# Kernel tuning notes

Hardware: AMD Instinct MI355X
Metric: run time of the kernel (lower is better)

The kernel has to match this reference:

```python
import math
import jax, jax.numpy as jnp
from jax import lax
import numpy as np

C_CURV = 0.01
CHUNK = 1024
EPS = 1e-15
TANH_CLIP = 1.0 - 1e-6


def safe_norm(x):
    return jnp.maximum(jnp.linalg.norm(x, axis=-1, keepdims=True), EPS)


def exp_map_zero(v, c):
    sqrt_c = math.sqrt(c)
    vn = safe_norm(v)
    return jnp.tanh(sqrt_c * vn) * v / (sqrt_c * vn)


def log_map_zero(y, c):
    sqrt_c = math.sqrt(c)
    yn = safe_norm(y)
    arg = jnp.clip(sqrt_c * yn, -TANH_CLIP, TANH_CLIP)
    return jnp.arctanh(arg) * y / (sqrt_c * yn)


def mobius_add(x, y, c):
    x2 = jnp.sum(x * x, axis=-1, keepdims=True)
    y2 = jnp.sum(y * y, axis=-1, keepdims=True)
    xy = jnp.sum(x * y, axis=-1, keepdims=True)
    num = (1.0 + 2.0 * c * xy + c * y2) * x + (1.0 - c * x2) * y
    den = 1.0 + 2.0 * c * xy + (c * c) * x2 * y2
    return num / jnp.maximum(den, EPS)


def givens_rotation(x, angles):
    # x: (B, d), angles: (B, d/2)
    x1 = x[:, 0::2]
    x2 = x[:, 1::2]
    cos_a = jnp.cos(angles)
    sin_a = jnp.sin(angles)
    out1 = cos_a * x1 - sin_a * x2
    out2 = sin_a * x1 + cos_a * x2
    # interleave back: stack on axis 2 then flatten
    return jnp.stack([out1, out2], axis=2).reshape(x.shape[0], x.shape[1])


def setup_inputs() -> dict:
    key = jax.random.key(0)
    k1, k2, k3, k4, k5, k6 = jax.random.split(key, 6)
    E, R, D, B = 40960, 480, 512, 128
    # keep entity points well inside the Poincare ball of curvature c
    entity_embedding = 0.05 * jax.random.normal(k1, (E, D), dtype=jnp.float32)
    rel_embedding = jax.random.normal(k2, (R, D), dtype=jnp.float32)  # unused, interface parity
    rel_rot = jax.random.uniform(k3, (R, D // 2), dtype=jnp.float32,
                                 minval=-math.pi, maxval=math.pi)
    rel_trans = jax.random.uniform(k4, (R, D), dtype=jnp.float32,
                                   minval=-0.001, maxval=0.001)
    entity_bias = jnp.zeros((E,), dtype=jnp.float32)
    triplets = jax.random.randint(k6, (B, 3), 0, R, dtype=jnp.int64)
    return {
        "entity_embedding": entity_embedding,
        "rel_embedding": rel_embedding,
        "rel_rot": rel_rot,
        "rel_trans": rel_trans,
        "entity_bias": entity_bias,
        "triplets": triplets,
    }


def reference(entity_embedding, rel_embedding, rel_rot, rel_trans, entity_bias, triplets):
    c = C_CURV
    E, D = entity_embedding.shape
    r_idx = triplets[:, 1]
    s_emb = entity_embedding[triplets[:, 0]]            # (B, d)
    s_tan = log_map_zero(s_emb, c)
    rot_s_tan = givens_rotation(s_tan, rel_rot[r_idx])
    rot_s = exp_map_zero(rot_s_tan, c)
    t_r = exp_map_zero(rel_trans[r_idx], c)
    query = mobius_add(rot_s, t_r, c)                   # (B, d)

    n_chunks = E // CHUNK
    ent_chunks = entity_embedding.reshape(n_chunks, CHUNK, D)
    bias_chunks = entity_bias.reshape(n_chunks, CHUNK)

    neg_q = -query[:, None, :]                          # (B, 1, d)

    def body(_, inp):
        cand, b = inp                                   # (CHUNK, d), (CHUNK,)
        diff = mobius_add(neg_q, cand[None, :, :], c)   # (B, CHUNK, d)
        dist_sq = jnp.sum(diff * diff, axis=-1)         # (B, CHUNK)
        return None, -dist_sq + b[None, :]

    _, chunks = lax.scan(body, None, (ent_chunks, bias_chunks))  # (n_chunks, B, CHUNK)
    scores = jnp.transpose(chunks, (1, 0, 2)).reshape(query.shape[0], E)
    scores = scores + entity_bias[triplets[:, 0]][:, None]
    return scores
```

## Files before the change

### kernel.cpp

```cpp
#include <hip/hip_runtime.h>
#include <math.h>

#define C_C   0.01f
#define SQC   0.1f
#define EPSF  1e-15f
#define TCLIP (1.0f - 1e-6f)

typedef short short8 __attribute__((ext_vector_type(8)));
typedef float f32x4  __attribute__((ext_vector_type(4)));

__device__ __forceinline__ float wred(float v) {
#pragma unroll
    for (int off = 32; off > 0; off >>= 1) v += __shfl_xor(v, off, 64);
    return v;
}

__device__ __forceinline__ float dot4(const float4& a, const float4& b) {
    return a.x * b.x + a.y * b.y + a.z * b.z + a.w * b.w;
}

__device__ __forceinline__ unsigned int f2bf(float f) {
    unsigned int u = __float_as_uint(f);
    u += 0x7fffu + ((u >> 16) & 1u);
    return u >> 16;
}
__device__ __forceinline__ unsigned int pk2(float a, float b) {
    return f2bf(a) | (f2bf(b) << 16);
}

__global__ __launch_bounds__(64)
void build_queries(const float* __restrict__ ent,
                   const float* __restrict__ rrot,
                   const float* __restrict__ rtrans,
                   const float* __restrict__ ebias,
                   const int* __restrict__ trip,
                   unsigned short* __restrict__ qb,
                   float* __restrict__ q2buf,
                   float* __restrict__ sbbuf)
{
    const int b    = blockIdx.x;
    const int lane = threadIdx.x;
    const int t0   = trip[b * 3 + 0];
    const int r    = trip[b * 3 + 1];

    const float* srow = ent + (size_t)t0 * 512;
    float4 s0 = *(const float4*)(srow + 4 * lane);
    float4 s1 = *(const float4*)(srow + 256 + 4 * lane);

    float ss = dot4(s0, s0) + dot4(s1, s1);
    ss = wred(ss);
    float yn  = fmaxf(sqrtf(ss), EPSF);
    float arg = fminf(SQC * yn, TCLIP);
    float fl  = atanhf(arg) / (SQC * yn);

    const float* arow = rrot + (size_t)r * 256;
    float2 a01 = *(const float2*)(arow + 2 * lane);
    float2 a23 = *(const float2*)(arow + 128 + 2 * lane);
    float c0, n0, c1, n1, c2, n2, c3, n3;
    sincosf(a01.x, &n0, &c0);
    sincosf(a01.y, &n1, &c1);
    sincosf(a23.x, &n2, &c2);
    sincosf(a23.y, &n3, &c3);

    float t0x = s0.x * fl, t0y = s0.y * fl, t0z = s0.z * fl, t0w = s0.w * fl;
    float t1x = s1.x * fl, t1y = s1.y * fl, t1z = s1.z * fl, t1w = s1.w * fl;

    float4 r0, r1;
    r0.x = c0 * t0x - n0 * t0y;  r0.y = n0 * t0x + c0 * t0y;
    r0.z = c1 * t0z - n1 * t0w;  r0.w = n1 * t0z + c1 * t0w;
    r1.x = c2 * t1x - n2 * t1y;  r1.y = n2 * t1x + c2 * t1y;
    r1.z = c3 * t1z - n3 * t1w;  r1.w = n3 * t1z + c3 * t1w;

    float vv = dot4(r0, r0) + dot4(r1, r1);
    vv = wred(vv);
    float vn = fmaxf(sqrtf(vv), EPSF);
    float fx = tanhf(SQC * vn) / (SQC * vn);

    const float* trow = rtrans + (size_t)r * 512;
    float4 u0 = *(const float4*)(trow + 4 * lane);
    float4 u1 = *(const float4*)(trow + 256 + 4 * lane);
    float tt = dot4(u0, u0) + dot4(u1, u1);
    float rt = dot4(r0, u0) + dot4(r1, u1);
    tt = wred(tt);
    rt = wred(rt);
    float tn = fmaxf(sqrtf(tt), EPSF);
    float fy = tanhf(SQC * tn) / (SQC * tn);

    float x2 = fx * fx * vv;
    float y2 = fy * fy * tt;
    float xy = fx * fy * rt;
    float ca  = 1.0f + 2.0f * C_C * xy + C_C * y2;
    float cb  = 1.0f - C_C * x2;
    float den = fmaxf(1.0f + 2.0f * C_C * xy + C_C * C_C * x2 * y2, EPSF);
    float inv = 1.0f / den;

    float4 q0, q1;
    q0.x = (ca * fx * r0.x + cb * fy * u0.x) * inv;
    q0.y = (ca * fx * r0.y + cb * fy * u0.y) * inv;
    q0.z = (ca * fx * r0.z + cb * fy * u0.z) * inv;
    q0.w = (ca * fx * r0.w + cb * fy * u0.w) * inv;
    q1.x = (ca * fx * r1.x + cb * fy * u1.x) * inv;
    q1.y = (ca * fx * r1.y + cb * fy * u1.y) * inv;
    q1.z = (ca * fx * r1.z + cb * fy * u1.z) * inv;
    q1.w = (ca * fx * r1.w + cb * fy * u1.w) * inv;

    float qq = dot4(q0, q0) + dot4(q1, q1);
    qq = wred(qq);

    unsigned short* qrow = qb + (size_t)b * 512;
    uint2 h0, h1;
    h0.x = pk2(q0.x, q0.y);  h0.y = pk2(q0.z, q0.w);
    h1.x = pk2(q1.x, q1.y);  h1.y = pk2(q1.z, q1.w);
    *(uint2*)(qrow + 4 * lane)       = h0;
    *(uint2*)(qrow + 256 + 4 * lane) = h1;
    if (lane == 0) {
        q2buf[b] = qq;
        sbbuf[b] = ebias[t0];
    }
}

__global__ __launch_bounds__(256)
void score_mfma(const float* __restrict__ ent,
                const float* __restrict__ ebias,
                const unsigned short* __restrict__ qb,
                const float* __restrict__ q2buf,
                const float* __restrict__ sbbuf,
                float* __restrict__ out, int E)
{
    __shared__ unsigned short qs[128 * 64];
    __shared__ unsigned short es[64 * 64];
    __shared__ float e2s[64];

    const int tid  = threadIdx.x;
    const int lane = tid & 63;
    const int wid  = tid >> 6;
    const int wr   = wid >> 1;
    const int wc   = wid & 1;
    const int e0   = blockIdx.x * 64;

    f32x4 acc[4][2];
#pragma unroll
    for (int mi = 0; mi < 4; ++mi)
#pragma unroll
        for (int nj = 0; nj < 2; ++nj) acc[mi][nj] = (f32x4)0.0f;

    const int erow0 = tid >> 3;
    const int ekc   = tid & 7;
    float e2p0 = 0.0f, e2p1 = 0.0f;

    for (int k0 = 0; k0 < 512; k0 += 64) {
        __syncthreads();
#pragma unroll
        for (int i = 0; i < 4; ++i) {
            int ci  = i * 256 + tid;
            int row = ci >> 3, kc = ci & 7;
            uint4 v = *(const uint4*)(qb + (size_t)row * 512 + k0 + kc * 8);
            int off = row * 128 + ((kc * 16) ^ ((row & 7) << 4));
            *(uint4*)((char*)qs + off) = v;
        }
        {
            const float* src = ent + (size_t)(e0 + erow0) * 512 + k0 + ekc * 8;
            float4 f0 = *(const float4*)(src);
            float4 f1 = *(const float4*)(src + 4);
            e2p0 += dot4(f0, f0) + dot4(f1, f1);
            uint4 p = { pk2(f0.x, f0.y), pk2(f0.z, f0.w),
                        pk2(f1.x, f1.y), pk2(f1.z, f1.w) };
            int off = erow0 * 128 + ((ekc * 16) ^ ((erow0 & 7) << 4));
            *(uint4*)((char*)es + off) = p;
        }
        {
            int row = erow0 + 32;
            const float* src = ent + (size_t)(e0 + row) * 512 + k0 + ekc * 8;
            float4 f0 = *(const float4*)(src);
            float4 f1 = *(const float4*)(src + 4);
            e2p1 += dot4(f0, f0) + dot4(f1, f1);
            uint4 p = { pk2(f0.x, f0.y), pk2(f0.z, f0.w),
                        pk2(f1.x, f1.y), pk2(f1.z, f1.w) };
            int off = row * 128 + ((ekc * 16) ^ ((row & 7) << 4));
            *(uint4*)((char*)es + off) = p;
        }
        __syncthreads();

#pragma unroll
        for (int ks = 0; ks < 2; ++ks) {
            const int kb = (ks * 32 + (lane >> 4) * 8) * 2;
            short8 a[4], bfr[2];
#pragma unroll
            for (int mi = 0; mi < 4; ++mi) {
                int row = wr * 64 + mi * 16 + (lane & 15);
                a[mi] = *(const short8*)((const char*)qs +
                         row * 128 + (kb ^ ((row & 7) << 4)));
            }
#pragma unroll
            for (int nj = 0; nj < 2; ++nj) {
                int row = wc * 32 + nj * 16 + (lane & 15);
                bfr[nj] = *(const short8*)((const char*)es +
                           row * 128 + (kb ^ ((row & 7) << 4)));
            }
#pragma unroll
            for (int mi = 0; mi < 4; ++mi)
#pragma unroll
                for (int nj = 0; nj < 2; ++nj)
                    acc[mi][nj] = __builtin_amdgcn_mfma_f32_16x16x32_bf16(
                        a[mi], bfr[nj], acc[mi][nj], 0, 0, 0);
        }
    }

    e2p0 += __shfl_xor(e2p0, 1, 64);
    e2p0 += __shfl_xor(e2p0, 2, 64);
    e2p0 += __shfl_xor(e2p0, 4, 64);
    e2p1 += __shfl_xor(e2p1, 1, 64);
    e2p1 += __shfl_xor(e2p1, 2, 64);
    e2p1 += __shfl_xor(e2p1, 4, 64);
    if ((tid & 7) == 0) {
        e2s[erow0]      = e2p0;
        e2s[erow0 + 32] = e2p1;
    }
    __syncthreads();

    float e2v[2], bev[2];
#pragma unroll
    for (int nj = 0; nj < 2; ++nj) {
        int ecol = wc * 32 + nj * 16 + (lane & 15);
        e2v[nj] = e2s[ecol];
        bev[nj] = ebias[e0 + ecol];
    }
#pragma unroll
    for (int mi = 0; mi < 4; ++mi) {
        const int qbase = wr * 64 + mi * 16 + (lane >> 4) * 4;
        float q2a[4], sba[4];
#pragma unroll
        for (int r = 0; r < 4; ++r) {
            q2a[r] = q2buf[qbase + r];
            sba[r] = sbbuf[qbase + r];
        }
#pragma unroll
        for (int nj = 0; nj < 2; ++nj) {
            const int ecol = e0 + wc * 32 + nj * 16 + (lane & 15);
            const float e2 = e2v[nj];
            const float be = bev[nj];
#pragma unroll
            for (int r = 0; r < 4; ++r) {
                float q2  = q2a[r];
                float xy  = -acc[mi][nj][r];
                float ca  = 1.0f + 2.0f * C_C * xy + C_C * e2;
                float cb  = 1.0f - C_C * q2;
                float den = fmaxf(1.0f + 2.0f * C_C * xy + C_C * C_C * q2 * e2, EPSF);
                float id2 = 1.0f / (den * den);
                float dist = (ca * ca * q2 + 2.0f * ca * cb * xy + cb * cb * e2) * id2;
                out[(size_t)(qbase + r) * E + ecol] = sba[r] + be - dist;
            }
        }
    }
}

extern "C" void kernel_launch(void* const* d_in, const int* in_sizes, int n_in,
                              void* d_out, int out_size, void* d_ws, size_t ws_size,
                              hipStream_t stream) {
    const float* ent    = (const float*)d_in[0];
    const float* rrot   = (const float*)d_in[2];
    const float* rtrans = (const float*)d_in[3];
    const float* ebias  = (const float*)d_in[4];
    const int*   trip   = (const int*)d_in[5];
    float* out = (float*)d_out;

    const int B = in_sizes[5] / 3;
    const int E = in_sizes[0] / 512;

    unsigned short* qb = (unsigned short*)d_ws;
    float* q2buf = (float*)(qb + (size_t)B * 512);
    float* sbbuf = q2buf + B;

    build_queries<<<B, 64, 0, stream>>>(ent, rrot, rtrans, ebias, trip,
                                        qb, q2buf, sbbuf);
    score_mfma<<<E / 64, 256, 0, stream>>>(ent, ebias, qb, q2buf, sbbuf, out, E);
}
```

Measured before the change: 145.5 us.

## Double-buffer LDS tiles with register prefetch and widen entity tile to 128

The scoring kernel now processes 128 entities per block instead of 64 and double-buffers the query and entity tiles in LDS. Global loads for the next K-slice are issued into registers before the MFMA work on the current slice, then stored to the alternate buffer. This halves redundant query tile loads and aims to hide global latency behind the matrix math. In exchange, LDS use and registers rise and the grid halves, which may reduce occupancy and CU fill.

```diff
diff --git a/kernel.cpp b/kernel.cpp
--- a/kernel.cpp
+++ b/kernel.cpp
@@ -127,101 +127,107 @@
                 const float* __restrict__ sbbuf,
                 float* __restrict__ out, int E)
 {
-    __shared__ unsigned short qs[128 * 64];
-    __shared__ unsigned short es[64 * 64];
-    __shared__ float e2s[64];
+    __shared__ unsigned short qs[2][128 * 64];
+    __shared__ unsigned short es[2][128 * 64];
+    __shared__ float e2s[128];
 
     const int tid  = threadIdx.x;
     const int lane = tid & 63;
     const int wid  = tid >> 6;
     const int wr   = wid >> 1;
     const int wc   = wid & 1;
-    const int e0   = blockIdx.x * 64;
-
-    f32x4 acc[4][2];
+    const int e0   = blockIdx.x * 128;
+
+    const int row  = tid >> 1;
+    const int half = tid & 1;
+
+    f32x4 acc[4][4];
 #pragma unroll
     for (int mi = 0; mi < 4; ++mi)
 #pragma unroll
-        for (int nj = 0; nj < 2; ++nj) acc[mi][nj] = (f32x4)0.0f;
-
-    const int erow0 = tid >> 3;
-    const int ekc   = tid & 7;
-    float e2p0 = 0.0f, e2p1 = 0.0f;
-
-    for (int k0 = 0; k0 < 512; k0 += 64) {
+        for (int nj = 0; nj < 4; ++nj) acc[mi][nj] = (f32x4)0.0f;
+
+    uint4  qreg[4];
+    float4 ereg[8];
+    float  e2p = 0.0f;
+
+    const unsigned short* qsrc0 = qb + (size_t)row * 512 + half * 32;
+    const float*          esrc0 = ent + (size_t)(e0 + row) * 512 + half * 32;
+
+#define LOAD_TILES(K0)                                                    \
+    {                                                                     \
+        const unsigned short* qsrc = qsrc0 + (K0);                        \
+        _Pragma("unroll")                                                 \
+        for (int c = 0; c < 4; ++c) qreg[c] = *(const uint4*)(qsrc + c * 8); \
+        const float* esrc = esrc0 + (K0);                                 \
+        _Pragma("unroll")                                                 \
+        for (int c = 0; c < 8; ++c) ereg[c] = *(const float4*)(esrc + c * 4); \
+    }
+
+#define STORE_TILES(BUF)                                                  \
+    {                                                                     \
+        _Pragma("unroll")                                                 \
+        for (int c = 0; c < 4; ++c) {                                     \
+            int off = row * 128 + ((((half * 4 + c) * 16)) ^ ((row & 7) << 4)); \
+            *(uint4*)((char*)qs[BUF] + off) = qreg[c];                    \
+        }                                                                 \
+        _Pragma("unroll")                                                 \
+        for (int p = 0; p < 4; ++p) {                                     \
+            float4 f0 = ereg[2 * p], f1 = ereg[2 * p + 1];                \
+            e2p += dot4(f0, f0) + dot4(f1, f1);                           \
+            uint4 pkd = { pk2(f0.x, f0.y), pk2(f0.z, f0.w),               \
+                          pk2(f1.x, f1.y), pk2(f1.z, f1.w) };             \
+            int off = row * 128 + ((((half * 4 + p) * 16)) ^ ((row & 7) << 4)); \
+            *(uint4*)((char*)es[BUF] + off) = pkd;                        \
+        }                                                                 \
+    }
+
+    LOAD_TILES(0);
+    STORE_TILES(0);
+    __syncthreads();
+
+    int cur = 0;
+#pragma unroll
+    for (int t = 0; t < 8; ++t) {
+        if (t < 7) LOAD_TILES((t + 1) * 64);
+
+#pragma unroll
+        for (int ks = 0; ks < 2; ++ks) {
+            const int kb = (ks * 4 + (lane >> 4)) * 16;
+            short8 a[4], b[4];
+#pragma unroll
+            for (int mi = 0; mi < 4; ++mi) {
+                int r = wr * 64 + mi * 16 + (lane & 15);
+                a[mi] = *(const short8*)((const char*)qs[cur] +
+                         r * 128 + (kb ^ ((r & 7) << 4)));
+            }
+#pragma unroll
+            for (int nj = 0; nj < 4; ++nj) {
+                int r = wc * 64 + nj * 16 + (lane & 15);
+                b[nj] = *(const short8*)((const char*)es[cur] +
+                         r * 128 + (kb ^ ((r & 7) << 4)));
+            }
+#pragma unroll
+            for (int mi = 0; mi < 4; ++mi)
+#pragma unroll
+                for (int nj = 0; nj < 4; ++nj)
+                    acc[mi][nj] = __builtin_amdgcn_mfma_f32_16x16x32_bf16(
+                        a[mi], b[nj], acc[mi][nj], 0, 0, 0);
+        }
+
+        if (t < 7) STORE_TILES(cur ^ 1);
         __syncthreads();
-#pragma unroll
-        for (int i = 0; i < 4; ++i) {
-            int ci  = i * 256 + tid;
-            int row = ci >> 3, kc = ci & 7;
-            uint4 v = *(const uint4*)(qb + (size_t)row * 512 + k0 + kc * 8);
-            int off = row * 128 + ((kc * 16) ^ ((row & 7) << 4));
-            *(uint4*)((char*)qs + off) = v;
-        }
-        {
-            const float* src = ent + (size_t)(e0 + erow0) * 512 + k0 + ekc * 8;
-            float4 f0 = *(const float4*)(src);
-            float4 f1 = *(const float4*)(src + 4);
-            e2p0 += dot4(f0, f0) + dot4(f1, f1);
-            uint4 p = { pk2(f0.x, f0.y), pk2(f0.z, f0.w),
-                        pk2(f1.x, f1.y), pk2(f1.z, f1.w) };
-            int off = erow0 * 128 + ((ekc * 16) ^ ((erow0 & 7) << 4));
-            *(uint4*)((char*)es + off) = p;
-        }
-        {
-            int row = erow0 + 32;
-            const float* src = ent + (size_t)(e0 + row) * 512 + k0 + ekc * 8;
-            float4 f0 = *(const float4*)(src);
-            float4 f1 = *(const float4*)(src + 4);
-            e2p1 += dot4(f0, f0) + dot4(f1, f1);
-            uint4 p = { pk2(f0.x, f0.y), pk2(f0.z, f0.w),
-                        pk2(f1.x, f1.y), pk2(f1.z, f1.w) };
-            int off = row * 128 + ((ekc * 16) ^ ((row & 7) << 4));
-            *(uint4*)((char*)es + off) = p;
-        }
-        __syncthreads();
-
-#pragma unroll
-        for (int ks = 0; ks < 2; ++ks) {
-            const int kb = (ks * 32 + (lane >> 4) * 8) * 2;
-            short8 a[4], bfr[2];
-#pragma unroll
-            for (int mi = 0; mi < 4; ++mi) {
-                int row = wr * 64 + mi * 16 + (lane & 15);
-                a[mi] = *(const short8*)((const char*)qs +
-                         row * 128 + (kb ^ ((row & 7) << 4)));
-            }
-#pragma unroll
-            for (int nj = 0; nj < 2; ++nj) {
-                int row = wc * 32 + nj * 16 + (lane & 15);
-                bfr[nj] = *(const short8*)((const char*)es +
-                           row * 128 + (kb ^ ((row & 7) << 4)));
-            }
-#pragma unroll
-            for (int mi = 0; mi < 4; ++mi)
-#pragma unroll
-                for (int nj = 0; nj < 2; ++nj)
-                    acc[mi][nj] = __builtin_amdgcn_mfma_f32_16x16x32_bf16(
-                        a[mi], bfr[nj], acc[mi][nj], 0, 0, 0);
-        }
-    }
-
-    e2p0 += __shfl_xor(e2p0, 1, 64);
-    e2p0 += __shfl_xor(e2p0, 2, 64);
-    e2p0 += __shfl_xor(e2p0, 4, 64);
-    e2p1 += __shfl_xor(e2p1, 1, 64);
-    e2p1 += __shfl_xor(e2p1, 2, 64);
-    e2p1 += __shfl_xor(e2p1, 4, 64);
-    if ((tid & 7) == 0) {
-        e2s[erow0]      = e2p0;
-        e2s[erow0 + 32] = e2p1;
-    }
+        cur ^= 1;
+    }
+
+    e2p += __shfl_xor(e2p, 1, 64);
+    if (half == 0) e2s[row] = e2p;
     __syncthreads();
 
-    float e2v[2], bev[2];
-#pragma unroll
-    for (int nj = 0; nj < 2; ++nj) {
-        int ecol = wc * 32 + nj * 16 + (lane & 15);
+    float e2v[4], bev[4];
+#pragma unroll
+    for (int nj = 0; nj < 4; ++nj) {
+        int ecol = wc * 64 + nj * 16 + (lane & 15);
         e2v[nj] = e2s[ecol];
         bev[nj] = ebias[e0 + ecol];
     }
@@ -235,8 +241,8 @@
             sba[r] = sbbuf[qbase + r];
         }
 #pragma unroll
-        for (int nj = 0; nj < 2; ++nj) {
-            const int ecol = e0 + wc * 32 + nj * 16 + (lane & 15);
+        for (int nj = 0; nj < 4; ++nj) {
+            const int ecol = e0 + wc * 64 + nj * 16 + (lane & 15);
             const float e2 = e2v[nj];
             const float be = bev[nj];
 #pragma unroll
@@ -252,6 +258,8 @@
             }
         }
     }
+#undef LOAD_TILES
+#undef STORE_TILES
 }
 
 extern "C" void kernel_launch(void* const* d_in, const int* in_sizes, int n_in,
@@ -273,5 +281,5 @@
 
     build_queries<<<B, 64, 0, stream>>>(ent, rrot, rtrans, ebias, trip,
                                         qb, q2buf, sbbuf);
-    score_mfma<<<E / 64, 256, 0, stream>>>(ent, ebias, qb, q2buf, sbbuf, out, E);
-}
+    score_mfma<<<E / 128, 256, 0, stream>>>(ent, ebias, qb, q2buf, sbbuf, out, E);
+}
```

Result: slower. 155.2 us (+6.7%).
